# Kernel tuning notes

Hardware: AMD Instinct MI355X
Metric: run time of the kernel (lower is better)

Reference implementation:

```python
import math
from functools import lru_cache
import numpy as np
import jax, jax.numpy as jnp

# ---------------- CG coefficient precompute (mirrors torch-gauge) ----------------

def _fact(n):
    return math.factorial(n)


def _cg_complex(j1, m1, j2, m2, j, m):
    """Clebsch-Gordan coefficient <j1 m1 j2 m2 | j m> for integer l (Racah formula)."""
    if m1 + m2 != m:
        return 0.0
    if j < abs(j1 - j2) or j > j1 + j2:
        return 0.0
    pre = math.sqrt((2 * j + 1) * _fact(j1 + j2 - j) * _fact(j1 - j2 + j)
                    * _fact(-j1 + j2 + j) / _fact(j1 + j2 + j + 1))
    pre *= math.sqrt(_fact(j1 + m1) * _fact(j1 - m1) * _fact(j2 + m2)
                     * _fact(j2 - m2) * _fact(j + m) * _fact(j - m))
    kmin = max(0, j2 - j - m1, j1 + m2 - j)
    kmax = min(j1 + j2 - j, j1 - m1, j2 + m2)
    s = 0.0
    for k in range(kmin, kmax + 1):
        s += (-1) ** k / (_fact(k) * _fact(j1 + j2 - j - k) * _fact(j1 - m1 - k)
                          * _fact(j2 + m2 - k) * _fact(j - j2 + m1 + k) * _fact(j - j1 - m2 + k))
    return pre * s


def _csh_to_rsh(l):
    """Unitary complex->real spherical harmonics transform, columns = real m."""
    A = np.zeros((2 * l + 1, 2 * l + 1), dtype=np.complex128)
    s2 = 1.0 / math.sqrt(2.0)
    for m in range(-l, l + 1):
        if m < 0:
            A[l + m, l + m] = 1j * s2
            A[l - m, l + m] = -1j * ((-1) ** m) * s2
        elif m == 0:
            A[l, l] = 1.0
        else:
            A[l + m, l + m] = ((-1) ** m) * s2
            A[l - m, l + m] = s2
    return A


@lru_cache(maxsize=None)
def _rsh_cg_compact(j1, j2, j):
    """Real-SH CG coefficients in compact [4, nnz] form: (m1, m2, m, coeff)."""
    csh = np.zeros((2 * j1 + 1, 2 * j2 + 1, 2 * j + 1))
    for m1 in range(-j1, j1 + 1):
        for m2 in range(-j2, j2 + 1):
            m = m1 + m2
            if -j <= m <= j:
                csh[j1 + m1, j2 + m2, j + m] = _cg_complex(j1, m1, j2, m2, j, m)
    rsh = np.einsum('abc,ai,bj,ck->ijk', csh.astype(np.complex128),
                    _csh_to_rsh(j1), _csh_to_rsh(j2), np.conj(_csh_to_rsh(j)))
    rsh = np.real(rsh * ((-1j) ** (j1 + j2 + j)))
    m1s, m2s, ms = np.meshgrid(np.arange(-j1, j1 + 1), np.arange(-j2, j2 + 1),
                               np.arange(-j, j + 1), indexing='ij')
    mask = np.abs(rsh) > 1e-12
    return np.stack([m1s[mask], m2s[mask], ms[mask], rsh[mask]], axis=0)


def _build_coupler(md1, md2, parity=0, overlap_out=True, trunc_in=True):
    """Replicates CGCoupler._init_params: builds cg_tilde and gather/scatter indices."""
    md1 = np.asarray(md1, dtype=np.int64)
    md2 = np.asarray(md2, dtype=np.int64)
    md_in = np.stack([md1, md2])
    max_n_out = np.maximum(md1, md2)
    L = md_in.shape[1]
    n_irreps = np.arange(L) * 2 + 1
    off_in = np.cumsum(md_in * n_irreps[None, :], axis=1)
    off_in = np.concatenate([np.zeros((2, 1), dtype=np.int64), off_in[:, :-1]], axis=1)
    max_l = L - 1
    metadata_out = np.zeros_like(max_n_out)
    valid = []
    for lout in range(max_l + 1):
        for l1 in range(max_l + 1):
            for l2 in range(max_l + 1):
                cp = (-1) ** (lout + l1 + l2)
                if parity != 0 and parity != cp:
                    continue
                if l1 + l2 < lout or abs(l1 - l2) > lout:
                    continue
                if trunc_in:
                    if l1 + l2 > max_l:
                        continue
                    deg = int(min(md_in[0, l1], md_in[1, l2], max_n_out[l1 + l2]))
                else:
                    deg = int(min(md_in[0, l1], md_in[1, l2], max_n_out[lout]))
                if not overlap_out:
                    metadata_out[lout] += deg
                elif deg > metadata_out[lout]:
                    metadata_out[lout] = deg
                if deg > 0:
                    valid.append((lout, l1, l2, deg))
    off_out = np.cumsum(metadata_out * n_irreps)
    off_out = np.concatenate([[0], off_out[:-1]]).astype(np.int64)
    cg_tilde, r1, r2, ro = [], [], [], []
    ns_off, lout_last = 0, 0
    for lout, l1, l2, deg in valid:
        if lout > lout_last:
            ns_off = 0
        src = _rsh_cg_compact(l1, l2, lout)  # [4, nnz]
        seg = np.repeat(src, deg, axis=1)    # repeat_interleave along columns
        ns = np.tile(np.arange(deg), src.shape[1])
        r1.append(off_in[0, l1] + (seg[0] + l1) * md_in[0, l1] + ns)
        r2.append(off_in[1, l2] + (seg[1] + l2) * md_in[1, l2] + ns)
        ro.append(off_out[lout] + (seg[2] + lout) * metadata_out[lout] + ns_off + ns)
        cg_tilde.append(seg[3])
        if not overlap_out:
            ns_off += deg
        lout_last = lout
    out_dim = int(np.sum(metadata_out * n_irreps))
    return (np.concatenate(cg_tilde).astype(np.float32),
            np.concatenate(r1).astype(np.int64),
            np.concatenate(r2).astype(np.int64),
            np.concatenate(ro).astype(np.int64),
            out_dim)


METADATA = [64, 64, 32, 32]  # lmax=3, rep_dim = 64 + 192 + 160 + 224 = 640
N_BATCH = 16384


def setup_inputs() -> dict:
    key = jax.random.key(0)
    k1, k2 = jax.random.split(key)
    cg, r1, r2, ro, out_dim = _build_coupler(METADATA, METADATA,
                                             parity=0, overlap_out=True, trunc_in=True)
    rep_dim = int(np.sum(np.asarray(METADATA) * (np.arange(len(METADATA)) * 2 + 1)))
    x1 = jax.random.normal(k1, (N_BATCH, rep_dim), dtype=jnp.float32)
    x2 = jax.random.normal(k2, (N_BATCH, rep_dim), dtype=jnp.float32)
    return {
        'x1': x1, 'x2': x2,
        'cg_tilde': jnp.asarray(cg),
        'repids_in1': jnp.asarray(r1),
        'repids_in2': jnp.asarray(r2),
        'repids_out': jnp.asarray(ro),
        'out_dim': out_dim,
    }


def reference(x1, x2, cg_tilde, repids_in1, repids_in2, repids_out, out_dim):
    # gather -> multiply by CG coefficients -> scatter-add along the rep dim
    out_tilde = x1[:, repids_in1] * x2[:, repids_in2] * cg_tilde[None, :]  # [N, M]
    out = jnp.zeros((x1.shape[0], out_dim), dtype=x1.dtype)
    return out.at[:, repids_out].add(out_tilde)
```

## Files before the change

### kernel.cpp

```cpp
#include <hip/hip_runtime.h>
#include <cstddef>


#define BLOCK 256


constexpr double cfact(int n) { double r = 1; for (int i = 2; i <= n; ++i) r *= i; return r; }

constexpr double csqrt_(double x) {
    if (x <= 0) return 0;
    double g = x;
    for (int i = 0; i < 80; ++i) g = 0.5 * (g + x / g);
    return g;
}

constexpr double cg_complex(int j1, int m1, int j2, int m2, int j, int m) {
    if (m1 + m2 != m) return 0;
    int dj = (j1 - j2 < 0) ? (j2 - j1) : (j1 - j2);
    if (j < dj || j > j1 + j2) return 0;
    double pre = csqrt_((2 * j + 1) * cfact(j1 + j2 - j) * cfact(j1 - j2 + j)
                        * cfact(-j1 + j2 + j) / cfact(j1 + j2 + j + 1));
    pre *= csqrt_(cfact(j1 + m1) * cfact(j1 - m1) * cfact(j2 + m2)
                  * cfact(j2 - m2) * cfact(j + m) * cfact(j - m));
    int kmin = 0;
    if (j2 - j - m1 > kmin) kmin = j2 - j - m1;
    if (j1 + m2 - j > kmin) kmin = j1 + m2 - j;
    int kmax = j1 + j2 - j;
    if (j1 - m1 < kmax) kmax = j1 - m1;
    if (j2 + m2 < kmax) kmax = j2 + m2;
    double s = 0;
    for (int k = kmin; k <= kmax; ++k) {
        double t = 1.0 / (cfact(k) * cfact(j1 + j2 - j - k) * cfact(j1 - m1 - k)
                          * cfact(j2 + m2 - k) * cfact(j - j2 + m1 + k) * cfact(j - j1 - m2 + k));
        s += (k & 1) ? -t : t;
    }
    return pre * s;
}

struct CD { double re, im; };
constexpr CD cmul(CD a, CD b) { return {a.re * b.re - a.im * b.im, a.re * b.im + a.im * b.re}; }

constexpr CD A_ent(int l, int a, int col) {
    const double s2 = 0.70710678118654752440;
    int m = col - l, mp = a - l;
    if (m < 0) {
        double sgn = ((-m) & 1) ? -1.0 : 1.0;
        if (mp == m)  return {0.0, s2};
        if (mp == -m) return {0.0, -sgn * s2};
        return {0.0, 0.0};
    } else if (m == 0) {
        return (mp == 0) ? CD{1.0, 0.0} : CD{0.0, 0.0};
    } else {
        double sgn = (m & 1) ? -1.0 : 1.0;
        if (mp == m)  return {sgn * s2, 0.0};
        if (mp == -m) return {s2, 0.0};
        return {0.0, 0.0};
    }
}

constexpr double rsh_cg(int j1, int j2, int j, int i, int jj, int k) {
    double re = 0, im = 0;
    for (int m1 = -j1; m1 <= j1; ++m1)
        for (int m2 = -j2; m2 <= j2; ++m2) {
            int m = m1 + m2;
            if (m < -j || m > j) continue;
            double c = cg_complex(j1, m1, j2, m2, j, m);
            if (c == 0) continue;
            CD a1 = A_ent(j1, j1 + m1, i);
            CD a2 = A_ent(j2, j2 + m2, jj);
            CD a3 = A_ent(j, j + m, k);
            a3.im = -a3.im;
            CD p = cmul(cmul(a1, a2), a3);
            re += c * p.re;
            im += c * p.im;
        }
    int ph = (j1 + j2 + j) & 3;
    if (ph == 0) return re;
    if (ph == 1) return im;
    if (ph == 2) return -re;
    return -im;
}


template <int L1, int L2, int LO, int IDX, int NT>
__device__ __forceinline__ void terms_rec(const float* __restrict__ x1v,
                                          const float* __restrict__ x2v,
                                          float* __restrict__ acc) {
    if constexpr (IDX < NT) {
        constexpr int N2 = 2 * L2 + 1, NO = 2 * LO + 1;
        constexpr int u1 = IDX / (N2 * NO);
        constexpr int u2 = (IDX / NO) % N2;
        constexpr int uo = IDX % NO;
        constexpr double v = rsh_cg(L1, L2, LO, u1, u2, uo);
        constexpr float cgv = (v > 1e-12 || v < -1e-12) ? (float)v : 0.0f;
        constexpr int SB1 = (L1 == 0) ? 0 : (L1 == 1) ? 1 : (L1 == 2) ? 4 : 9;
        constexpr int SB2 = (L2 == 0) ? 0 : (L2 == 1) ? 1 : (L2 == 2) ? 4 : 9;
        constexpr int SBO = (LO == 0) ? 0 : (LO == 1) ? 1 : (LO == 2) ? 4 : 9;
        if constexpr (cgv != 0.0f) {
            acc[SBO + uo] += cgv * x1v[SB1 + u1] * x2v[SB2 + u2];
        }
        terms_rec<L1, L2, LO, IDX + 1, NT>(x1v, x2v, acc);
    }
}

template <int L1, int L2, int LO>
__device__ __forceinline__ void proc_block(const float* __restrict__ x1v,
                                           const float* __restrict__ x2v,
                                           float* __restrict__ acc) {
    terms_rec<L1, L2, LO, 0, (2 * L1 + 1) * (2 * L2 + 1) * (2 * LO + 1)>(x1v, x2v, acc);
}


__global__ __launch_bounds__(BLOCK) void cg_main_kernel(
    const float* __restrict__ x1, const float* __restrict__ x2,
    float* __restrict__ out, int N)
{
    const int gid  = blockIdx.x * BLOCK + threadIdx.x;
    const int wave = gid >> 6;
    const int lane = gid & 63;
    const int sub  = lane >> 5;
    const int t    = lane & 31;
    const int row  = wave * 2 + sub;
    if (row >= N) return;

    const float* p1 = x1 + (size_t)row * 640;
    const float* p2 = x2 + (size_t)row * 640;

    float x1t[16], x2t[16], acct[16];
    float x1u[4],  x2u[4],  accu[4];
#pragma unroll
    for (int i = 0; i < 16; ++i) acct[i] = 0.f;
#pragma unroll
    for (int i = 0; i < 4; ++i) accu[i] = 0.f;

    x1t[0] = p1[t];       x2t[0] = p2[t];
    x1u[0] = p1[t + 32];  x2u[0] = p2[t + 32];
#pragma unroll
    for (int u = 0; u < 3; ++u) {
        x1t[1 + u] = p1[64 + u * 64 + t];
        x2t[1 + u] = p2[64 + u * 64 + t];
        x1u[1 + u] = p1[64 + u * 64 + t + 32];
        x2u[1 + u] = p2[64 + u * 64 + t + 32];
    }
#pragma unroll
    for (int u = 0; u < 5; ++u) {
        x1t[4 + u] = p1[256 + u * 32 + t];
        x2t[4 + u] = p2[256 + u * 32 + t];
    }
#pragma unroll
    for (int u = 0; u < 7; ++u) {
        x1t[9 + u] = p1[416 + u * 32 + t];
        x2t[9 + u] = p2[416 + u * 32 + t];
    }

    proc_block<0, 0, 0>(x1t, x2t, acct);
    proc_block<0, 1, 1>(x1t, x2t, acct);
    proc_block<1, 0, 1>(x1t, x2t, acct);
    proc_block<0, 0, 0>(x1u, x2u, accu);
    proc_block<0, 1, 1>(x1u, x2u, accu);
    proc_block<1, 0, 1>(x1u, x2u, accu);

    proc_block<1, 1, 0>(x1t, x2t, acct);
    proc_block<1, 1, 1>(x1t, x2t, acct);
    proc_block<1, 2, 1>(x1t, x2t, acct);
    proc_block<2, 1, 1>(x1t, x2t, acct);
    proc_block<0, 2, 2>(x1t, x2t, acct);
    proc_block<2, 0, 2>(x1t, x2t, acct);
    proc_block<1, 1, 2>(x1t, x2t, acct);
    proc_block<1, 2, 2>(x1t, x2t, acct);
    proc_block<2, 1, 2>(x1t, x2t, acct);
    proc_block<0, 3, 3>(x1t, x2t, acct);
    proc_block<3, 0, 3>(x1t, x2t, acct);
    proc_block<1, 2, 3>(x1t, x2t, acct);
    proc_block<2, 1, 3>(x1t, x2t, acct);

    float* po = out + (size_t)row * 640;
    __builtin_nontemporal_store(acct[0], po + t);
    __builtin_nontemporal_store(accu[0], po + t + 32);
#pragma unroll
    for (int u = 0; u < 3; ++u) {
        __builtin_nontemporal_store(acct[1 + u], po + 64 + u * 64 + t);
        __builtin_nontemporal_store(accu[1 + u], po + 64 + u * 64 + t + 32);
    }
#pragma unroll
    for (int u = 0; u < 5; ++u)
        __builtin_nontemporal_store(acct[4 + u], po + 256 + u * 32 + t);
#pragma unroll
    for (int u = 0; u < 7; ++u)
        __builtin_nontemporal_store(acct[9 + u], po + 416 + u * 32 + t);
}

extern "C" void kernel_launch(void* const* d_in, const int* in_sizes, int n_in,
                              void* d_out, int out_size, void* d_ws, size_t ws_size,
                              hipStream_t stream) {
    const float* x1 = (const float*)d_in[0];
    const float* x2 = (const float*)d_in[1];
    float* out = (float*)d_out;

    const int N = in_sizes[0] / 640;

    const int total_threads = N * 32;
    cg_main_kernel<<<(total_threads + BLOCK - 1) / BLOCK, BLOCK, 0, stream>>>(
        x1, x2, out, N);
}
```

Before: 124.7 us.

## Stage rows through LDS with vectorized 128-bit global loads and stores

Each block now copies 8 full rows of x1 and x2 into shared memory using float4 loads, computes from LDS, writes results back into LDS and then streams them out with float4 nontemporal stores. This replaces 32-bit strided per-thread global accesses with wide, fully contiguous transactions. The cost is 40KB of LDS per block, two barriers and extra LDS traffic, which may lower occupancy.

```diff
diff --git a/kernel.cpp b/kernel.cpp
--- a/kernel.cpp
+++ b/kernel.cpp
@@ -3,6 +3,9 @@
 
 
 #define BLOCK 256
+#define RPB 8
+
+typedef float f32x4 __attribute__((ext_vector_type(4)));
 
 
 constexpr double cfact(int n) { double r = 1; for (int i = 2; i <= n; ++i) r *= i; return r; }
@@ -115,79 +118,110 @@
     const float* __restrict__ x1, const float* __restrict__ x2,
     float* __restrict__ out, int N)
 {
-    const int gid  = blockIdx.x * BLOCK + threadIdx.x;
-    const int wave = gid >> 6;
-    const int lane = gid & 63;
-    const int sub  = lane >> 5;
-    const int t    = lane & 31;
-    const int row  = wave * 2 + sub;
-    if (row >= N) return;
-
-    const float* p1 = x1 + (size_t)row * 640;
-    const float* p2 = x2 + (size_t)row * 640;
-
-    float x1t[16], x2t[16], acct[16];
-    float x1u[4],  x2u[4],  accu[4];
-#pragma unroll
-    for (int i = 0; i < 16; ++i) acct[i] = 0.f;
-#pragma unroll
-    for (int i = 0; i < 4; ++i) accu[i] = 0.f;
-
-    x1t[0] = p1[t];       x2t[0] = p2[t];
-    x1u[0] = p1[t + 32];  x2u[0] = p2[t + 32];
-#pragma unroll
-    for (int u = 0; u < 3; ++u) {
-        x1t[1 + u] = p1[64 + u * 64 + t];
-        x2t[1 + u] = p2[64 + u * 64 + t];
-        x1u[1 + u] = p1[64 + u * 64 + t + 32];
-        x2u[1 + u] = p2[64 + u * 64 + t + 32];
-    }
-#pragma unroll
-    for (int u = 0; u < 5; ++u) {
-        x1t[4 + u] = p1[256 + u * 32 + t];
-        x2t[4 + u] = p2[256 + u * 32 + t];
-    }
-#pragma unroll
-    for (int u = 0; u < 7; ++u) {
-        x1t[9 + u] = p1[416 + u * 32 + t];
-        x2t[9 + u] = p2[416 + u * 32 + t];
-    }
-
-    proc_block<0, 0, 0>(x1t, x2t, acct);
-    proc_block<0, 1, 1>(x1t, x2t, acct);
-    proc_block<1, 0, 1>(x1t, x2t, acct);
-    proc_block<0, 0, 0>(x1u, x2u, accu);
-    proc_block<0, 1, 1>(x1u, x2u, accu);
-    proc_block<1, 0, 1>(x1u, x2u, accu);
-
-    proc_block<1, 1, 0>(x1t, x2t, acct);
-    proc_block<1, 1, 1>(x1t, x2t, acct);
-    proc_block<1, 2, 1>(x1t, x2t, acct);
-    proc_block<2, 1, 1>(x1t, x2t, acct);
-    proc_block<0, 2, 2>(x1t, x2t, acct);
-    proc_block<2, 0, 2>(x1t, x2t, acct);
-    proc_block<1, 1, 2>(x1t, x2t, acct);
-    proc_block<1, 2, 2>(x1t, x2t, acct);
-    proc_block<2, 1, 2>(x1t, x2t, acct);
-    proc_block<0, 3, 3>(x1t, x2t, acct);
-    proc_block<3, 0, 3>(x1t, x2t, acct);
-    proc_block<1, 2, 3>(x1t, x2t, acct);
-    proc_block<2, 1, 3>(x1t, x2t, acct);
-
-    float* po = out + (size_t)row * 640;
-    __builtin_nontemporal_store(acct[0], po + t);
-    __builtin_nontemporal_store(accu[0], po + t + 32);
-#pragma unroll
-    for (int u = 0; u < 3; ++u) {
-        __builtin_nontemporal_store(acct[1 + u], po + 64 + u * 64 + t);
-        __builtin_nontemporal_store(accu[1 + u], po + 64 + u * 64 + t + 32);
-    }
-#pragma unroll
-    for (int u = 0; u < 5; ++u)
-        __builtin_nontemporal_store(acct[4 + u], po + 256 + u * 32 + t);
-#pragma unroll
-    for (int u = 0; u < 7; ++u)
-        __builtin_nontemporal_store(acct[9 + u], po + 416 + u * 32 + t);
+    __shared__ f32x4 lds1v[RPB * 160];
+    __shared__ f32x4 lds2v[RPB * 160];
+    float* lds1 = (float*)lds1v;
+    float* lds2 = (float*)lds2v;
+
+    const int tid = threadIdx.x;
+    const int r0  = blockIdx.x * RPB;
+    const int nrows = (N - r0 < RPB) ? (N - r0) : RPB;
+    const int nq = nrows * 160;
+    const size_t base = (size_t)r0 * 640;
+
+    const f32x4* __restrict__ s1 = (const f32x4*)(x1 + base);
+    const f32x4* __restrict__ s2 = (const f32x4*)(x2 + base);
+#pragma unroll
+    for (int i = 0; i < 5; ++i) {
+        const int idx = i * BLOCK + tid;
+        if (idx < nq) {
+            lds1v[idx] = s1[idx];
+            lds2v[idx] = s2[idx];
+        }
+    }
+    __syncthreads();
+
+    const int lr = tid >> 5;
+    const int t  = tid & 31;
+
+    if (lr < nrows) {
+        const float* p1 = lds1 + lr * 640;
+        const float* p2 = lds2 + lr * 640;
+
+        float x1t[16], x2t[16], acct[16];
+        float x1u[4],  x2u[4],  accu[4];
+#pragma unroll
+        for (int i = 0; i < 16; ++i) acct[i] = 0.f;
+#pragma unroll
+        for (int i = 0; i < 4; ++i) accu[i] = 0.f;
+
+        x1t[0] = p1[t];       x2t[0] = p2[t];
+        x1u[0] = p1[t + 32];  x2u[0] = p2[t + 32];
+#pragma unroll
+        for (int u = 0; u < 3; ++u) {
+            x1t[1 + u] = p1[64 + u * 64 + t];
+            x2t[1 + u] = p2[64 + u * 64 + t];
+            x1u[1 + u] = p1[64 + u * 64 + t + 32];
+            x2u[1 + u] = p2[64 + u * 64 + t + 32];
+        }
+#pragma unroll
+        for (int u = 0; u < 5; ++u) {
+            x1t[4 + u] = p1[256 + u * 32 + t];
+            x2t[4 + u] = p2[256 + u * 32 + t];
+        }
+#pragma unroll
+        for (int u = 0; u < 7; ++u) {
+            x1t[9 + u] = p1[416 + u * 32 + t];
+            x2t[9 + u] = p2[416 + u * 32 + t];
+        }
+
+        proc_block<0, 0, 0>(x1t, x2t, acct);
+        proc_block<0, 1, 1>(x1t, x2t, acct);
+        proc_block<1, 0, 1>(x1t, x2t, acct);
+        proc_block<0, 0, 0>(x1u, x2u, accu);
+        proc_block<0, 1, 1>(x1u, x2u, accu);
+        proc_block<1, 0, 1>(x1u, x2u, accu);
+
+        proc_block<1, 1, 0>(x1t, x2t, acct);
+        proc_block<1, 1, 1>(x1t, x2t, acct);
+        proc_block<1, 2, 1>(x1t, x2t, acct);
+        proc_block<2, 1, 1>(x1t, x2t, acct);
+        proc_block<0, 2, 2>(x1t, x2t, acct);
+        proc_block<2, 0, 2>(x1t, x2t, acct);
+        proc_block<1, 1, 2>(x1t, x2t, acct);
+        proc_block<1, 2, 2>(x1t, x2t, acct);
+        proc_block<2, 1, 2>(x1t, x2t, acct);
+        proc_block<0, 3, 3>(x1t, x2t, acct);
+        proc_block<3, 0, 3>(x1t, x2t, acct);
+        proc_block<1, 2, 3>(x1t, x2t, acct);
+        proc_block<2, 1, 3>(x1t, x2t, acct);
+
+        float* po = lds1 + lr * 640;
+        po[t]      = acct[0];
+        po[t + 32] = accu[0];
+#pragma unroll
+        for (int u = 0; u < 3; ++u) {
+            po[64 + u * 64 + t]      = acct[1 + u];
+            po[64 + u * 64 + t + 32] = accu[1 + u];
+        }
+#pragma unroll
+        for (int u = 0; u < 5; ++u)
+            po[256 + u * 32 + t] = acct[4 + u];
+#pragma unroll
+        for (int u = 0; u < 7; ++u)
+            po[416 + u * 32 + t] = acct[9 + u];
+    }
+    __syncthreads();
+
+    f32x4* __restrict__ o4 = (f32x4*)(out + base);
+#pragma unroll
+    for (int i = 0; i < 5; ++i) {
+        const int idx = i * BLOCK + tid;
+        if (idx < nq) {
+            f32x4 v = lds1v[idx];
+            __builtin_nontemporal_store(v, o4 + idx);
+        }
+    }
 }
 
 extern "C" void kernel_launch(void* const* d_in, const int* in_sizes, int n_in,
@@ -198,8 +232,6 @@
     float* out = (float*)d_out;
 
     const int N = in_sizes[0] / 640;
-
-    const int total_threads = N * 32;
-    cg_main_kernel<<<(total_threads + BLOCK - 1) / BLOCK, BLOCK, 0, stream>>>(
-        x1, x2, out, N);
-}
+    const int blocks = (N + RPB - 1) / RPB;
+    cg_main_kernel<<<blocks, BLOCK, 0, stream>>>(x1, x2, out, N);
+}
```

Result: no change. 126.2 us (median of 2 runs) (+1.2%).

## Stage rows through double-buffered LDS with vectorized loads and register prefetch

Applied to the files above, without the earlier changes.

Each 64-thread block now handles four two-row tiles in sequence. It loads each tile with coalesced 16-byte vector loads and stages it in double-buffered shared memory, while the next tile's global loads are issued into registers before the current tile is computed. This aims to improve load vectorization and overlap memory latency with compute. In exchange there are far fewer waves in flight, extra LDS traffic, and no barrier, which is safe only because each block is a single wavefront. Odd N would leave the last row unprocessed.

```diff
diff --git a/kernel.cpp b/kernel.cpp
--- a/kernel.cpp
+++ b/kernel.cpp
@@ -2,7 +2,10 @@
 #include <cstddef>
 
 
-#define BLOCK 256
+#define BLOCK 64
+#define TPB 4
+
+typedef float f32x4 __attribute__((ext_vector_type(4)));
 
 
 constexpr double cfact(int n) { double r = 1; for (int i = 2; i <= n; ++i) r *= i; return r; }
@@ -115,79 +118,112 @@
     const float* __restrict__ x1, const float* __restrict__ x2,
     float* __restrict__ out, int N)
 {
-    const int gid  = blockIdx.x * BLOCK + threadIdx.x;
-    const int wave = gid >> 6;
-    const int lane = gid & 63;
-    const int sub  = lane >> 5;
+    __shared__ f32x4 bufA1[320], bufA2[320], bufB1[320], bufB2[320];
+
+    const int lane = threadIdx.x;
+    const int lr   = lane >> 5;
     const int t    = lane & 31;
-    const int row  = wave * 2 + sub;
-    if (row >= N) return;
-
-    const float* p1 = x1 + (size_t)row * 640;
-    const float* p2 = x2 + (size_t)row * 640;
-
-    float x1t[16], x2t[16], acct[16];
-    float x1u[4],  x2u[4],  accu[4];
-#pragma unroll
-    for (int i = 0; i < 16; ++i) acct[i] = 0.f;
-#pragma unroll
-    for (int i = 0; i < 4; ++i) accu[i] = 0.f;
-
-    x1t[0] = p1[t];       x2t[0] = p2[t];
-    x1u[0] = p1[t + 32];  x2u[0] = p2[t + 32];
-#pragma unroll
-    for (int u = 0; u < 3; ++u) {
-        x1t[1 + u] = p1[64 + u * 64 + t];
-        x2t[1 + u] = p2[64 + u * 64 + t];
-        x1u[1 + u] = p1[64 + u * 64 + t + 32];
-        x2u[1 + u] = p2[64 + u * 64 + t + 32];
-    }
-#pragma unroll
-    for (int u = 0; u < 5; ++u) {
-        x1t[4 + u] = p1[256 + u * 32 + t];
-        x2t[4 + u] = p2[256 + u * 32 + t];
-    }
-#pragma unroll
-    for (int u = 0; u < 7; ++u) {
-        x1t[9 + u] = p1[416 + u * 32 + t];
-        x2t[9 + u] = p2[416 + u * 32 + t];
-    }
-
-    proc_block<0, 0, 0>(x1t, x2t, acct);
-    proc_block<0, 1, 1>(x1t, x2t, acct);
-    proc_block<1, 0, 1>(x1t, x2t, acct);
-    proc_block<0, 0, 0>(x1u, x2u, accu);
-    proc_block<0, 1, 1>(x1u, x2u, accu);
-    proc_block<1, 0, 1>(x1u, x2u, accu);
-
-    proc_block<1, 1, 0>(x1t, x2t, acct);
-    proc_block<1, 1, 1>(x1t, x2t, acct);
-    proc_block<1, 2, 1>(x1t, x2t, acct);
-    proc_block<2, 1, 1>(x1t, x2t, acct);
-    proc_block<0, 2, 2>(x1t, x2t, acct);
-    proc_block<2, 0, 2>(x1t, x2t, acct);
-    proc_block<1, 1, 2>(x1t, x2t, acct);
-    proc_block<1, 2, 2>(x1t, x2t, acct);
-    proc_block<2, 1, 2>(x1t, x2t, acct);
-    proc_block<0, 3, 3>(x1t, x2t, acct);
-    proc_block<3, 0, 3>(x1t, x2t, acct);
-    proc_block<1, 2, 3>(x1t, x2t, acct);
-    proc_block<2, 1, 3>(x1t, x2t, acct);
-
-    float* po = out + (size_t)row * 640;
-    __builtin_nontemporal_store(acct[0], po + t);
-    __builtin_nontemporal_store(accu[0], po + t + 32);
-#pragma unroll
-    for (int u = 0; u < 3; ++u) {
-        __builtin_nontemporal_store(acct[1 + u], po + 64 + u * 64 + t);
-        __builtin_nontemporal_store(accu[1 + u], po + 64 + u * 64 + t + 32);
-    }
-#pragma unroll
-    for (int u = 0; u < 5; ++u)
-        __builtin_nontemporal_store(acct[4 + u], po + 256 + u * 32 + t);
-#pragma unroll
-    for (int u = 0; u < 7; ++u)
-        __builtin_nontemporal_store(acct[9 + u], po + 416 + u * 32 + t);
+
+    const int ntiles = N >> 1;
+    const int tile0  = blockIdx.x * TPB;
+    if (tile0 >= ntiles) return;
+    const int ntl = (ntiles - tile0 < TPB) ? (ntiles - tile0) : TPB;
+
+    f32x4 r1[5], r2[5];
+
+    {
+        const f32x4* __restrict__ g1 = (const f32x4*)(x1 + (size_t)tile0 * 1280);
+        const f32x4* __restrict__ g2 = (const f32x4*)(x2 + (size_t)tile0 * 1280);
+#pragma unroll
+        for (int i = 0; i < 5; ++i) { r1[i] = g1[i * 64 + lane]; r2[i] = g2[i * 64 + lane]; }
+#pragma unroll
+        for (int i = 0; i < 5; ++i) { bufA1[i * 64 + lane] = r1[i]; bufA2[i * 64 + lane] = r2[i]; }
+    }
+
+    for (int tt = 0; tt < ntl; ++tt) {
+        const int tile = tile0 + tt;
+        const bool has_next = (tt + 1 < ntl);
+
+        if (has_next) {
+            const f32x4* __restrict__ g1 = (const f32x4*)(x1 + (size_t)(tile + 1) * 1280);
+            const f32x4* __restrict__ g2 = (const f32x4*)(x2 + (size_t)(tile + 1) * 1280);
+#pragma unroll
+            for (int i = 0; i < 5; ++i) { r1[i] = g1[i * 64 + lane]; r2[i] = g2[i * 64 + lane]; }
+        }
+
+        const float* p1 = (const float*)((tt & 1) ? bufB1 : bufA1) + lr * 640;
+        const float* p2 = (const float*)((tt & 1) ? bufB2 : bufA2) + lr * 640;
+
+        float x1t[16], x2t[16], acct[16];
+        float x1u[4],  x2u[4],  accu[4];
+#pragma unroll
+        for (int i = 0; i < 16; ++i) acct[i] = 0.f;
+#pragma unroll
+        for (int i = 0; i < 4; ++i) accu[i] = 0.f;
+
+        x1t[0] = p1[t];       x2t[0] = p2[t];
+        x1u[0] = p1[t + 32];  x2u[0] = p2[t + 32];
+#pragma unroll
+        for (int u = 0; u < 3; ++u) {
+            x1t[1 + u] = p1[64 + u * 64 + t];
+            x2t[1 + u] = p2[64 + u * 64 + t];
+            x1u[1 + u] = p1[64 + u * 64 + t + 32];
+            x2u[1 + u] = p2[64 + u * 64 + t + 32];
+        }
+#pragma unroll
+        for (int u = 0; u < 5; ++u) {
+            x1t[4 + u] = p1[256 + u * 32 + t];
+            x2t[4 + u] = p2[256 + u * 32 + t];
+        }
+#pragma unroll
+        for (int u = 0; u < 7; ++u) {
+            x1t[9 + u] = p1[416 + u * 32 + t];
+            x2t[9 + u] = p2[416 + u * 32 + t];
+        }
+
+        proc_block<0, 0, 0>(x1t, x2t, acct);
+        proc_block<0, 1, 1>(x1t, x2t, acct);
+        proc_block<1, 0, 1>(x1t, x2t, acct);
+        proc_block<0, 0, 0>(x1u, x2u, accu);
+        proc_block<0, 1, 1>(x1u, x2u, accu);
+        proc_block<1, 0, 1>(x1u, x2u, accu);
+
+        proc_block<1, 1, 0>(x1t, x2t, acct);
+        proc_block<1, 1, 1>(x1t, x2t, acct);
+        proc_block<1, 2, 1>(x1t, x2t, acct);
+        proc_block<2, 1, 1>(x1t, x2t, acct);
+        proc_block<0, 2, 2>(x1t, x2t, acct);
+        proc_block<2, 0, 2>(x1t, x2t, acct);
+        proc_block<1, 1, 2>(x1t, x2t, acct);
+        proc_block<1, 2, 2>(x1t, x2t, acct);
+        proc_block<2, 1, 2>(x1t, x2t, acct);
+        proc_block<0, 3, 3>(x1t, x2t, acct);
+        proc_block<3, 0, 3>(x1t, x2t, acct);
+        proc_block<1, 2, 3>(x1t, x2t, acct);
+        proc_block<2, 1, 3>(x1t, x2t, acct);
+
+        float* po = out + (size_t)(tile * 2 + lr) * 640;
+        __builtin_nontemporal_store(acct[0], po + t);
+        __builtin_nontemporal_store(accu[0], po + t + 32);
+#pragma unroll
+        for (int u = 0; u < 3; ++u) {
+            __builtin_nontemporal_store(acct[1 + u], po + 64 + u * 64 + t);
+            __builtin_nontemporal_store(accu[1 + u], po + 64 + u * 64 + t + 32);
+        }
+#pragma unroll
+        for (int u = 0; u < 5; ++u)
+            __builtin_nontemporal_store(acct[4 + u], po + 256 + u * 32 + t);
+#pragma unroll
+        for (int u = 0; u < 7; ++u)
+            __builtin_nontemporal_store(acct[9 + u], po + 416 + u * 32 + t);
+
+        if (has_next) {
+            f32x4* l1 = (tt & 1) ? bufA1 : bufB1;
+            f32x4* l2 = (tt & 1) ? bufA2 : bufB2;
+#pragma unroll
+            for (int i = 0; i < 5; ++i) { l1[i * 64 + lane] = r1[i]; l2[i * 64 + lane] = r2[i]; }
+        }
+    }
 }
 
 extern "C" void kernel_launch(void* const* d_in, const int* in_sizes, int n_in,
@@ -198,8 +234,7 @@
     float* out = (float*)d_out;
 
     const int N = in_sizes[0] / 640;
-
-    const int total_threads = N * 32;
-    cg_main_kernel<<<(total_threads + BLOCK - 1) / BLOCK, BLOCK, 0, stream>>>(
-        x1, x2, out, N);
-}
+    const int ntiles = N >> 1;
+    const int blocks = (ntiles + TPB - 1) / TPB;
+    cg_main_kernel<<<blocks, BLOCK, 0, stream>>>(x1, x2, out, N);
+}
```

After: 130.6 us. +4.7%, slower.
